# Optimization experiments

Measured on AMD Instinct MI355X. Metric: run time of the kernel, lower is better.

Reference implementation:

```python
import jax, jax.numpy as jnp
import numpy as np

B, T, NM = 128, 2048, 8  # batch, nSteps, nMaxwell


def setup_inputs() -> dict:
    key = jax.random.key(0)
    k1, k2, k3 = jax.random.split(key, 3)
    S_e = jax.random.normal(k1, (B, T, 3, 3), dtype=jnp.float32)
    # strictly increasing times per batch element
    dt = jax.random.uniform(k2, (B, T), minval=0.01, maxval=0.1, dtype=jnp.float32)
    t = jnp.cumsum(dt, axis=1)
    # [tau_1..tau_nM, g_infy, g_1..g_nM] -> last dim 2*NM + 1
    PronyParams = jax.random.uniform(k3, (B, T, 2 * NM + 1), minval=0.1, maxval=1.0, dtype=jnp.float32)
    return {"S_e": S_e, "t": t, "PronyParams": PronyParams}


def reference(S_e, t, PronyParams):
    """Viscoelastic 2nd Piola-Kirchhoff stress via recursive Prony update.

    S_e:         [B, T, 3, 3] instantaneous elastic stress
    t:           [B, T] time
    PronyParams: [B, T, 2*nM+1] (relaxation times tau then coefficients g)
    Returns (S, S_infy, Q_sum), each [B, T, 3, 3].
    """
    nM = PronyParams.shape[-1] // 2
    tau = PronyParams[..., :nM]                      # [B,T,nM]
    g = PronyParams[..., nM:]                        # [B,T,nM+1]
    g = g / jnp.sum(g, axis=-1, keepdims=True)
    g_infy = g[..., 0:1]                             # [B,T,1]
    g_i = g[..., 1:]                                 # [B,T,nM]

    Bsz = S_e.shape[0]
    # time-major scan inputs
    xs = (
        jnp.swapaxes(t, 0, 1),      # [T,B]
        jnp.swapaxes(S_e, 0, 1),    # [T,B,3,3]
        jnp.swapaxes(tau, 0, 1),    # [T,B,nM]
        jnp.swapaxes(g_i, 0, 1),    # [T,B,nM]
    )
    init = (
        jnp.zeros((Bsz, nM, 3, 3), S_e.dtype),  # Q_0
        -t[:, 1],                                # t_prev (as in original initializer)
        jnp.zeros((Bsz, 3, 3), S_e.dtype),       # S_prev
        tau[:, 0],
        g_i[:, 0],
    )

    def step(carry, x):
        Q_p, t_p, S_p, tau_p, g_p = carry
        t_c, S_c, tau_c, g_c = x
        g_bar = 0.5 * (g_c + g_p)                 # [B,nM]
        tau_bar = 0.5 * (tau_c + tau_p)           # [B,nM]
        dt = (t_c - t_p)[:, None]                 # [B,1]
        e = jnp.exp(-0.5 * dt / tau_bar)          # exp(-dt/(2 tau_bar))
        term1 = (e * e)[..., None, None]          # exp(-dt/tau_bar), [B,nM,1,1]
        term2 = (e * g_bar)[..., None, None]      # [B,nM,1,1]
        dS = (S_c - S_p)[:, None]                 # [B,1,3,3]
        Q = term1 * Q_p + term2 * dS              # [B,nM,3,3]
        return (Q, t_c, S_c, tau_c, g_c), Q

    _, Qs = jax.lax.scan(step, init, xs)          # [T,B,nM,3,3]
    Q_sum = jnp.swapaxes(jnp.sum(Qs, axis=2), 0, 1)  # [B,T,3,3]
    S_infy = g_infy[..., None] * S_e              # [B,T,1,1] * [B,T,3,3]
    S = S_infy + Q_sum
    return (S, S_infy, Q_sum)
```

## Files before the change

kernel.cpp:

```cpp
#include <hip/hip_runtime.h>

#define T_LEN 2048
#define NMODE 8
#define NPP   17

template <int L, int G>
__global__ __launch_bounds__(256, 8)
void scanK(const float* __restrict__ Se,
           const float* __restrict__ tt,
           const float* __restrict__ pp,
           float* __restrict__ out,
           float* __restrict__ caT,
           float* __restrict__ agg,
           int B) {
    constexpr int NSTEP = G * L;
    constexpr int TILES = T_LEN / NSTEP;
    constexpr int RW    = NSTEP + 1;
    constexpr int NT    = 256;
    constexpr int SROW  = NSTEP + 4;
    constexpr int QT_SZ = 9 * SROW;
    constexpr int CA_K  = L * 8 + 4;
    constexpr int AC_K  = L * 16 + 4;
    constexpr int O_AC  = QT_SZ + G * CA_K;
    constexpr int OV_ZREL = 0;
    constexpr int OV_PP   = G * 72;
    constexpr int OV_R    = OV_PP + G * 8;
    constexpr int OV_P    = OV_R + G * 72;
    static_assert(OV_P + G * 8 <= G * AC_K, "overlay fits in AC region");
    constexpr int O_INV = O_AC + G * AC_K;
    constexpr int O_GI  = O_INV + RW;
    constexpr int TOTAL = O_GI + RW;
    static_assert(TOTAL * 4 <= 20480, "LDS must allow 8 blocks/CU");
    static_assert(L == 16, "epilogue uses t>>4 / t&15");

    __shared__ __align__(16) float sm[TOTAL];
    float* s_qT   = sm;
    float* s_ca   = sm + QT_SZ;
    float* s_AC   = sm + O_AC;
    float* s_Zrel = sm + O_AC + OV_ZREL;
    float* s_Pp   = sm + O_AC + OV_PP;
    float* s_R    = sm + O_AC + OV_R;
    float* s_P    = sm + O_AC + OV_P;
    float* s_inv  = sm + O_INV;
    float* s_gi   = sm + O_GI;

    const int tid = threadIdx.x;
    const int b    = blockIdx.x / TILES;
    const int tile = blockIdx.x % TILES;

    const int base = tile * NSTEP;
    const int off  = (base == 0) ? 0 : 1;
    const int r0   = (base == 0) ? 0 : base - 1;

    const float* ppb = pp + ((size_t)b * T_LEN + r0) * NPP;
    const float* ttb = tt + (size_t)b * T_LEN + r0;

    for (int i = tid; i < RW; i += NT) {
        const float* gp = ppb + i * NPP + 8;
        float gs = 0.f;
        #pragma unroll
        for (int k = 0; k < 9; ++k) gs += gp[k];
        float iv = __builtin_amdgcn_rcpf(gs);
        s_inv[i] = iv;
        s_gi[i]  = gp[0] * iv;
    }
    __syncthreads();

    for (int i = tid; i < NSTEP * 8; i += NT) {
        int m  = i & 7;
        int ts = i >> 3;
        int rc = ts + off;
        bool first = (base == 0) && (ts == 0);
        int rp = first ? rc : rc - 1;
        float tau_c = ppb[rc * NPP + m];
        float tau_p = ppb[rp * NPP + m];
        float gqh_c = 0.5f * ppb[rc * NPP + 9 + m] * s_inv[rc];
        float gqh_p = 0.5f * ppb[rp * NPP + 9 + m] * s_inv[rp];
        float t_c = ttb[rc];
        float t_p = first ? -ttb[1] : ttb[rp];
        float ee  = __expf((t_p - t_c) * __builtin_amdgcn_rcpf(tau_c + tau_p));
        int kk = ts / L, sl = ts % L;
        s_AC[kk * AC_K + sl * 16 + m]     = ee * ee;
        s_AC[kk * AC_K + sl * 16 + 8 + m] = ee * (gqh_c + gqh_p);
    }
    __syncthreads();

    const size_t nOut = (size_t)B * T_LEN * 9;
    float* o1 = out + nOut + ((size_t)b * T_LEN + base) * 9;
    float* o2 = out + 2 * nOut + ((size_t)b * T_LEN + base) * 9;
    const float4* sv4 = (const float4*)(Se + ((size_t)b * T_LEN + base) * 9);

    float Q[8] = {0,0,0,0,0,0,0,0};
    float cumA_c = 1.f;
    if (tid < 72) {
        const int k = tid / 9;
        const int e = tid - k * 9;
        const float* Sg = Se + (size_t)b * T_LEN * 9 + e;
        const int gbase = base + k * L;

        float dS[L];
        {
            float prev = (base == 0 && k == 0) ? 0.f
                                               : Sg[(size_t)(gbase - 1) * 9];
            #pragma unroll
            for (int s = 0; s < L; ++s) {
                float cur = Sg[(size_t)(gbase + s) * 9];
                dS[s] = cur - prev;
                prev = cur;
            }
        }

        const float4* acp = (const float4*)(s_AC + k * AC_K);
        #pragma unroll
        for (int s = 0; s < L; ++s) {
            float4 a0 = acp[4*s], a1 = acp[4*s+1];
            float4 c0v = acp[4*s+2], c1v = acp[4*s+3];
            float d = dS[s];
            Q[0] = a0.x*Q[0] + c0v.x*d;  Q[1] = a0.y*Q[1] + c0v.y*d;
            Q[2] = a0.z*Q[2] + c0v.z*d;  Q[3] = a0.w*Q[3] + c0v.w*d;
            Q[4] = a1.x*Q[4] + c1v.x*d;  Q[5] = a1.y*Q[5] + c1v.y*d;
            Q[6] = a1.z*Q[6] + c1v.z*d;  Q[7] = a1.w*Q[7] + c1v.w*d;
            float qs = ((Q[0]+Q[1])+(Q[2]+Q[3])) + ((Q[4]+Q[5])+(Q[6]+Q[7]));
            s_qT[e * SROW + (k * L + s)] = qs;
        }
    } else if (tid < 192) {
        for (int i4 = tid - 72; i4 < NSTEP * 9 / 4; i4 += 120) {
            float4 sv = sv4[i4];
            int i = i4 * 4;
            float f0 = s_gi[(i    ) / 9 + off] * sv.x;
            float f1 = s_gi[(i + 1) / 9 + off] * sv.y;
            float f2 = s_gi[(i + 2) / 9 + off] * sv.z;
            float f3 = s_gi[(i + 3) / 9 + off] * sv.w;
            ((float4*)o1)[i4] = make_float4(f0, f1, f2, f3);
        }
    } else {
        const int u = tid - 192;
        const int k = u >> 3;
        const int m = u & 7;
        #pragma unroll
        for (int s = 0; s < L; ++s) {
            cumA_c *= s_AC[k * AC_K + s * 16 + m];
            s_ca[k * CA_K + s * 8 + m] = cumA_c;
        }
    }
    __syncthreads();

    if (tid < 72) {
        float4* r4 = (float4*)(s_R + 8 * tid);
        r4[0] = make_float4(Q[0], Q[1], Q[2], Q[3]);
        r4[1] = make_float4(Q[4], Q[5], Q[6], Q[7]);
    } else if (tid >= 192) {
        s_P[tid - 192] = cumA_c;
    }
    __syncthreads();

    if (tid < 72) {
        const int e = tid >> 3;
        const int m = tid & 7;
        float z = 0.f, pprod = 1.f;
        #pragma unroll
        for (int k = 0; k < G; ++k) {
            s_Zrel[k * 72 + tid] = z;
            if (e == 0) s_Pp[k * 8 + m] = pprod;
            float Pk = s_P[k * 8 + m];
            z = Pk * z + s_R[k * 72 + tid];
            pprod *= Pk;
        }
        if (tile != TILES - 1) {
            float* ap = agg + ((size_t)b * TILES + tile) * 80;
            ap[8 + tid] = z;
            if (e == 0) ap[m] = pprod;
        }
    }
    __syncthreads();

    {
        int k = tid >> 5;
        int s = (tid >> 1) & 15;
        int h = tid & 1;
        float4 cv = *(const float4*)(s_ca + k * CA_K + s * 8 + h * 4);
        float4 pv = *(const float4*)(s_Pp + k * 8 + h * 4);
        float4 ov = make_float4(cv.x*pv.x, cv.y*pv.y, cv.z*pv.z, cv.w*pv.w);
        *(float4*)(caT + (((size_t)b * T_LEN + base) + k * L + s) * 8 + h * 4)
            = ov;
    }

    for (int i4 = tid; i4 < NSTEP * 9 / 4; i4 += NT) {
        int i = i4 * 4;
        float q[4];
        #pragma unroll
        for (int j = 0; j < 4; ++j) {
            int idx = i + j;
            int t = idx / 9, e = idx - t * 9;
            int k = t >> 4, s = t & 15;
            const float4* ca4 = (const float4*)(s_ca + k * CA_K + s * 8);
            const float4* z4  = (const float4*)(s_Zrel + k * 72 + e * 8);
            float4 cA = ca4[0], cB = ca4[1];
            float4 zA = z4[0],  zB = z4[1];
            float cr = ((cA.x*zA.x + cA.y*zA.y) + (cA.z*zA.z + cA.w*zA.w))
                     + ((cB.x*zB.x + cB.y*zB.y) + (cB.z*zB.z + cB.w*zB.w));
            q[j] = s_qT[e * SROW + t] + cr;
        }
        ((float4*)o2)[i4] = make_float4(q[0], q[1], q[2], q[3]);
    }
}

template <int L, int G>
__global__ __launch_bounds__(256, 8)
void finishK(float* __restrict__ out,
             const float* __restrict__ caT,
             const float* __restrict__ agg,
             int B) {
    constexpr int NSTEP = G * L;
    constexpr int TILES = T_LEN / NSTEP;
    constexpr int NT    = 256;

    __shared__ __align__(16) float s_Z[80];
    __shared__ __align__(16) float s_ca[NSTEP * 8];

    const int tid  = threadIdx.x;
    const int b    = blockIdx.x / TILES;
    const int tile = blockIdx.x % TILES;
    const int base = tile * NSTEP;

    {
        const float4* c4 = (const float4*)(caT + ((size_t)b * T_LEN + base) * 8);
        for (int i = tid; i < NSTEP * 8 / 4; i += NT)
            ((float4*)s_ca)[i] = c4[i];
    }

    if (tid < 72) {
        const int m = tid & 7;
        float zin = 0.f;
        if (tile > 0) {
            const float* ab = agg + (size_t)b * TILES * 80;
            float Pv[TILES - 1], Rv[TILES - 1];
            #pragma unroll
            for (int j = 0; j < TILES - 1; ++j) {
                if (j < tile) {
                    Pv[j] = ab[j * 80 + m];
                    Rv[j] = ab[j * 80 + 8 + tid];
                }
            }
            #pragma unroll
            for (int j = 0; j < TILES - 1; ++j)
                if (j < tile) zin = Pv[j] * zin + Rv[j];
        }
        s_Z[tid] = zin;
    }
    __syncthreads();

    const size_t nOut = (size_t)B * T_LEN * 9;
    float* o0 = out + ((size_t)b * T_LEN + base) * 9;
    const float4* sf4 = (const float4*)(o0 + nOut);
    float4* s4 = (float4*)o0;
    float4* q4 = (float4*)(o0 + 2 * nOut);

    for (int i4 = tid; i4 < NSTEP * 9 / 4; i4 += NT) {
        float4 qv = q4[i4];
        float4 fv = sf4[i4];
        int i = i4 * 4;
        float corr[4];
        #pragma unroll
        for (int j = 0; j < 4; ++j) {
            int idx = i + j;
            int t = idx / 9, e = idx - t * 9;
            const float4* ca4 = (const float4*)(s_ca + t * 8);
            const float4* z4  = (const float4*)(s_Z + e * 8);
            float4 cA = ca4[0], cB = ca4[1];
            float4 zA = z4[0],  zB = z4[1];
            corr[j] = ((cA.x*zA.x + cA.y*zA.y) + (cA.z*zA.z + cA.w*zA.w))
                    + ((cB.x*zB.x + cB.y*zB.y) + (cB.z*zB.z + cB.w*zB.w));
        }
        float4 qn = make_float4(qv.x + corr[0], qv.y + corr[1],
                                qv.z + corr[2], qv.w + corr[3]);
        q4[i4] = qn;
        s4[i4] = make_float4(fv.x + qn.x, fv.y + qn.y,
                             fv.z + qn.z, fv.w + qn.w);
    }
}

extern "C" void kernel_launch(void* const* d_in, const int* in_sizes, int n_in,
                              void* d_out, int out_size, void* d_ws, size_t ws_size,
                              hipStream_t stream) {
    const float* Se = (const float*)d_in[0];
    const float* tt = (const float*)d_in[1];
    const float* pp = (const float*)d_in[2];
    float* out = (float*)d_out;

    int B = in_sizes[1] / T_LEN;

    constexpr int L = 16;
    constexpr int G = 8;
    constexpr int NSTEP = G * L;
    constexpr int TILES = T_LEN / NSTEP;

    float* caT = (float*)d_ws;
    float* agg = caT + (size_t)B * T_LEN * 8;

    scanK<L, G><<<B * TILES, dim3(256), 0, stream>>>(
        Se, tt, pp, out, caT, agg, B);
    finishK<L, G><<<B * TILES, dim3(256), 0, stream>>>(
        out, caT, agg, B);
}
```

Baseline: 98.73 us.

## Replace scan-then-fixup with aggregate-then-recompute two-pass scan

The first kernel now computes only per-tile aggregates (decay product and partial Q) for all tiles but the last, and writes nothing else. The second kernel takes the carry-in from those aggregates, recomputes the local scan and writes all three outputs once. This removes the caT workspace and the global round trip where the first kernel wrote Q_sum and S_infy and the second kernel read them back and rewrote them. The cost is doing the coefficient and exp computation and the local scan twice.

```diff
diff --git a/kernel.cpp b/kernel.cpp
--- a/kernel.cpp
+++ b/kernel.cpp
@@ -6,47 +6,31 @@
 
 template <int L, int G>
 __global__ __launch_bounds__(256, 8)
-void scanK(const float* __restrict__ Se,
-           const float* __restrict__ tt,
-           const float* __restrict__ pp,
-           float* __restrict__ out,
-           float* __restrict__ caT,
-           float* __restrict__ agg,
-           int B) {
+void aggK(const float* __restrict__ Se,
+          const float* __restrict__ tt,
+          const float* __restrict__ pp,
+          float* __restrict__ agg,
+          int B) {
     constexpr int NSTEP = G * L;
     constexpr int TILES = T_LEN / NSTEP;
     constexpr int RW    = NSTEP + 1;
     constexpr int NT    = 256;
-    constexpr int SROW  = NSTEP + 4;
-    constexpr int QT_SZ = 9 * SROW;
-    constexpr int CA_K  = L * 8 + 4;
     constexpr int AC_K  = L * 16 + 4;
-    constexpr int O_AC  = QT_SZ + G * CA_K;
-    constexpr int OV_ZREL = 0;
-    constexpr int OV_PP   = G * 72;
-    constexpr int OV_R    = OV_PP + G * 8;
-    constexpr int OV_P    = OV_R + G * 72;
-    static_assert(OV_P + G * 8 <= G * AC_K, "overlay fits in AC region");
-    constexpr int O_INV = O_AC + G * AC_K;
-    constexpr int O_GI  = O_INV + RW;
-    constexpr int TOTAL = O_GI + RW;
-    static_assert(TOTAL * 4 <= 20480, "LDS must allow 8 blocks/CU");
-    static_assert(L == 16, "epilogue uses t>>4 / t&15");
+    constexpr int OV_R  = 0;
+    constexpr int OV_P  = G * 72;
+    static_assert(OV_P + G * 8 <= G * AC_K, "overlay fits");
+    constexpr int O_INV = G * AC_K;
+    constexpr int TOTAL = O_INV + RW;
 
     __shared__ __align__(16) float sm[TOTAL];
-    float* s_qT   = sm;
-    float* s_ca   = sm + QT_SZ;
-    float* s_AC   = sm + O_AC;
-    float* s_Zrel = sm + O_AC + OV_ZREL;
-    float* s_Pp   = sm + O_AC + OV_PP;
-    float* s_R    = sm + O_AC + OV_R;
-    float* s_P    = sm + O_AC + OV_P;
-    float* s_inv  = sm + O_INV;
-    float* s_gi   = sm + O_GI;
-
-    const int tid = threadIdx.x;
-    const int b    = blockIdx.x / TILES;
-    const int tile = blockIdx.x % TILES;
+    float* s_AC  = sm;
+    float* s_R   = sm + OV_R;
+    float* s_P   = sm + OV_P;
+    float* s_inv = sm + O_INV;
+
+    const int tid  = threadIdx.x;
+    const int b    = blockIdx.x / (TILES - 1);
+    const int tile = blockIdx.x % (TILES - 1);
 
     const int base = tile * NSTEP;
     const int off  = (base == 0) ? 0 : 1;
@@ -60,9 +44,7 @@
         float gs = 0.f;
         #pragma unroll
         for (int k = 0; k < 9; ++k) gs += gp[k];
-        float iv = __builtin_amdgcn_rcpf(gs);
-        s_inv[i] = iv;
-        s_gi[i]  = gp[0] * iv;
+        s_inv[i] = __builtin_amdgcn_rcpf(gs);
     }
     __syncthreads();
 
@@ -85,9 +67,177 @@
     }
     __syncthreads();
 
+    float Q[8] = {0,0,0,0,0,0,0,0};
+    float cumA_c = 1.f;
+    if (tid < 72) {
+        const int k = tid / 9;
+        const int e = tid - k * 9;
+        const float* Sg = Se + (size_t)b * T_LEN * 9 + e;
+        const int gbase = base + k * L;
+
+        float dS[L];
+        {
+            float prev = (base == 0 && k == 0) ? 0.f
+                                               : Sg[(size_t)(gbase - 1) * 9];
+            #pragma unroll
+            for (int s = 0; s < L; ++s) {
+                float cur = Sg[(size_t)(gbase + s) * 9];
+                dS[s] = cur - prev;
+                prev = cur;
+            }
+        }
+
+        const float4* acp = (const float4*)(s_AC + k * AC_K);
+        #pragma unroll
+        for (int s = 0; s < L; ++s) {
+            float4 a0 = acp[4*s], a1 = acp[4*s+1];
+            float4 c0v = acp[4*s+2], c1v = acp[4*s+3];
+            float d = dS[s];
+            Q[0] = a0.x*Q[0] + c0v.x*d;  Q[1] = a0.y*Q[1] + c0v.y*d;
+            Q[2] = a0.z*Q[2] + c0v.z*d;  Q[3] = a0.w*Q[3] + c0v.w*d;
+            Q[4] = a1.x*Q[4] + c1v.x*d;  Q[5] = a1.y*Q[5] + c1v.y*d;
+            Q[6] = a1.z*Q[6] + c1v.z*d;  Q[7] = a1.w*Q[7] + c1v.w*d;
+        }
+    } else if (tid >= 192) {
+        const int u = tid - 192;
+        const int k = u >> 3;
+        const int m = u & 7;
+        #pragma unroll
+        for (int s = 0; s < L; ++s)
+            cumA_c *= s_AC[k * AC_K + s * 16 + m];
+    }
+    __syncthreads();
+
+    if (tid < 72) {
+        float4* r4 = (float4*)(s_R + 8 * tid);
+        r4[0] = make_float4(Q[0], Q[1], Q[2], Q[3]);
+        r4[1] = make_float4(Q[4], Q[5], Q[6], Q[7]);
+    } else if (tid >= 192) {
+        s_P[tid - 192] = cumA_c;
+    }
+    __syncthreads();
+
+    if (tid < 72) {
+        const int e = tid >> 3;
+        const int m = tid & 7;
+        float z = 0.f, pprod = 1.f;
+        #pragma unroll
+        for (int k = 0; k < G; ++k) {
+            float Pk = s_P[k * 8 + m];
+            z = Pk * z + s_R[k * 72 + tid];
+            pprod *= Pk;
+        }
+        float* ap = agg + ((size_t)b * TILES + tile) * 80;
+        ap[8 + tid] = z;
+        if (e == 0) ap[m] = pprod;
+    }
+}
+
+template <int L, int G>
+__global__ __launch_bounds__(256, 8)
+void finK(const float* __restrict__ Se,
+          const float* __restrict__ tt,
+          const float* __restrict__ pp,
+          float* __restrict__ out,
+          const float* __restrict__ agg,
+          int B) {
+    constexpr int NSTEP = G * L;
+    constexpr int TILES = T_LEN / NSTEP;
+    constexpr int RW    = NSTEP + 1;
+    constexpr int NT    = 256;
+    constexpr int SROW  = NSTEP + 4;
+    constexpr int QT_SZ = 9 * SROW;
+    constexpr int CA_K  = L * 8 + 4;
+    constexpr int AC_K  = L * 16 + 4;
+    constexpr int O_AC  = QT_SZ + G * CA_K;
+    constexpr int OV_R  = 0;
+    constexpr int OV_P  = G * 72;
+    constexpr int OV_Z  = OV_P + G * 8;
+    static_assert(OV_Z + G * 72 <= G * AC_K, "overlay fits");
+    constexpr int O_INV = O_AC + G * AC_K;
+    constexpr int O_GI  = O_INV + RW;
+    constexpr int O_ZIN = O_GI + RW;
+    constexpr int TOTAL = O_ZIN + 72;
+    static_assert(TOTAL * 4 <= 20480, "LDS must allow 8 blocks/CU");
+    static_assert(L == 16, "epilogue uses t>>4 / t&15");
+
+    __shared__ __align__(16) float sm[TOTAL];
+    float* s_qT  = sm;
+    float* s_ca  = sm + QT_SZ;
+    float* s_AC  = sm + O_AC;
+    float* s_R   = sm + O_AC + OV_R;
+    float* s_P   = sm + O_AC + OV_P;
+    float* s_Z   = sm + O_AC + OV_Z;
+    float* s_inv = sm + O_INV;
+    float* s_gi  = sm + O_GI;
+    float* s_Zin = sm + O_ZIN;
+
+    const int tid  = threadIdx.x;
+    const int b    = blockIdx.x / TILES;
+    const int tile = blockIdx.x % TILES;
+
+    const int base = tile * NSTEP;
+    const int off  = (base == 0) ? 0 : 1;
+    const int r0   = (base == 0) ? 0 : base - 1;
+
+    const float* ppb = pp + ((size_t)b * T_LEN + r0) * NPP;
+    const float* ttb = tt + (size_t)b * T_LEN + r0;
+
+    if (tid < 72) {
+        float zin = 0.f;
+        if (tile > 0) {
+            const int m = tid & 7;
+            const float* ab = agg + (size_t)b * TILES * 80;
+            float Pv[TILES - 1], Rv[TILES - 1];
+            #pragma unroll
+            for (int j = 0; j < TILES - 1; ++j) {
+                if (j < tile) {
+                    Pv[j] = ab[j * 80 + m];
+                    Rv[j] = ab[j * 80 + 8 + tid];
+                }
+            }
+            #pragma unroll
+            for (int j = 0; j < TILES - 1; ++j)
+                if (j < tile) zin = Pv[j] * zin + Rv[j];
+        }
+        s_Zin[tid] = zin;
+    } else {
+        int i = tid - 72;
+        if (i < RW) {
+            const float* gp = ppb + i * NPP + 8;
+            float gs = 0.f;
+            #pragma unroll
+            for (int k = 0; k < 9; ++k) gs += gp[k];
+            float iv = __builtin_amdgcn_rcpf(gs);
+            s_inv[i] = iv;
+            s_gi[i]  = gp[0] * iv;
+        }
+    }
+    __syncthreads();
+
+    for (int i = tid; i < NSTEP * 8; i += NT) {
+        int m  = i & 7;
+        int ts = i >> 3;
+        int rc = ts + off;
+        bool first = (base == 0) && (ts == 0);
+        int rp = first ? rc : rc - 1;
+        float tau_c = ppb[rc * NPP + m];
+        float tau_p = ppb[rp * NPP + m];
+        float gqh_c = 0.5f * ppb[rc * NPP + 9 + m] * s_inv[rc];
+        float gqh_p = 0.5f * ppb[rp * NPP + 9 + m] * s_inv[rp];
+        float t_c = ttb[rc];
+        float t_p = first ? -ttb[1] : ttb[rp];
+        float ee  = __expf((t_p - t_c) * __builtin_amdgcn_rcpf(tau_c + tau_p));
+        int kk = ts / L, sl = ts % L;
+        s_AC[kk * AC_K + sl * 16 + m]     = ee * ee;
+        s_AC[kk * AC_K + sl * 16 + 8 + m] = ee * (gqh_c + gqh_p);
+    }
+    __syncthreads();
+
     const size_t nOut = (size_t)B * T_LEN * 9;
-    float* o1 = out + nOut + ((size_t)b * T_LEN + base) * 9;
-    float* o2 = out + 2 * nOut + ((size_t)b * T_LEN + base) * 9;
+    float* o0 = out + ((size_t)b * T_LEN + base) * 9;
+    float* o1 = o0 + nOut;
+    float* o2 = o0 + 2 * nOut;
     const float4* sv4 = (const float4*)(Se + ((size_t)b * T_LEN + base) * 9);
 
     float Q[8] = {0,0,0,0,0,0,0,0};
@@ -155,128 +305,39 @@
     __syncthreads();
 
     if (tid < 72) {
-        const int e = tid >> 3;
         const int m = tid & 7;
-        float z = 0.f, pprod = 1.f;
+        float z = s_Zin[tid];
         #pragma unroll
         for (int k = 0; k < G; ++k) {
-            s_Zrel[k * 72 + tid] = z;
-            if (e == 0) s_Pp[k * 8 + m] = pprod;
-            float Pk = s_P[k * 8 + m];
-            z = Pk * z + s_R[k * 72 + tid];
-            pprod *= Pk;
-        }
-        if (tile != TILES - 1) {
-            float* ap = agg + ((size_t)b * TILES + tile) * 80;
-            ap[8 + tid] = z;
-            if (e == 0) ap[m] = pprod;
-        }
-    }
-    __syncthreads();
-
-    {
-        int k = tid >> 5;
-        int s = (tid >> 1) & 15;
-        int h = tid & 1;
-        float4 cv = *(const float4*)(s_ca + k * CA_K + s * 8 + h * 4);
-        float4 pv = *(const float4*)(s_Pp + k * 8 + h * 4);
-        float4 ov = make_float4(cv.x*pv.x, cv.y*pv.y, cv.z*pv.z, cv.w*pv.w);
-        *(float4*)(caT + (((size_t)b * T_LEN + base) + k * L + s) * 8 + h * 4)
-            = ov;
-    }
+            s_Z[k * 72 + tid] = z;
+            z = s_P[k * 8 + m] * z + s_R[k * 72 + tid];
+        }
+    }
+    __syncthreads();
 
     for (int i4 = tid; i4 < NSTEP * 9 / 4; i4 += NT) {
+        float4 sv = sv4[i4];
+        const float svc[4] = {sv.x, sv.y, sv.z, sv.w};
         int i = i4 * 4;
-        float q[4];
+        float q[4], f[4];
         #pragma unroll
         for (int j = 0; j < 4; ++j) {
             int idx = i + j;
             int t = idx / 9, e = idx - t * 9;
+            int rc = t + off;
             int k = t >> 4, s = t & 15;
             const float4* ca4 = (const float4*)(s_ca + k * CA_K + s * 8);
-            const float4* z4  = (const float4*)(s_Zrel + k * 72 + e * 8);
+            const float4* z4  = (const float4*)(s_Z + k * 72 + e * 8);
             float4 cA = ca4[0], cB = ca4[1];
             float4 zA = z4[0],  zB = z4[1];
             float cr = ((cA.x*zA.x + cA.y*zA.y) + (cA.z*zA.z + cA.w*zA.w))
                      + ((cB.x*zB.x + cB.y*zB.y) + (cB.z*zB.z + cB.w*zB.w));
             q[j] = s_qT[e * SROW + t] + cr;
+            f[j] = s_gi[rc] * svc[j];
         }
         ((float4*)o2)[i4] = make_float4(q[0], q[1], q[2], q[3]);
-    }
-}
-
-template <int L, int G>
-__global__ __launch_bounds__(256, 8)
-void finishK(float* __restrict__ out,
-             const float* __restrict__ caT,
-             const float* __restrict__ agg,
-             int B) {
-    constexpr int NSTEP = G * L;
-    constexpr int TILES = T_LEN / NSTEP;
-    constexpr int NT    = 256;
-
-    __shared__ __align__(16) float s_Z[80];
-    __shared__ __align__(16) float s_ca[NSTEP * 8];
-
-    const int tid  = threadIdx.x;
-    const int b    = blockIdx.x / TILES;
-    const int tile = blockIdx.x % TILES;
-    const int base = tile * NSTEP;
-
-    {
-        const float4* c4 = (const float4*)(caT + ((size_t)b * T_LEN + base) * 8);
-        for (int i = tid; i < NSTEP * 8 / 4; i += NT)
-            ((float4*)s_ca)[i] = c4[i];
-    }
-
-    if (tid < 72) {
-        const int m = tid & 7;
-        float zin = 0.f;
-        if (tile > 0) {
-            const float* ab = agg + (size_t)b * TILES * 80;
-            float Pv[TILES - 1], Rv[TILES - 1];
-            #pragma unroll
-            for (int j = 0; j < TILES - 1; ++j) {
-                if (j < tile) {
-                    Pv[j] = ab[j * 80 + m];
-                    Rv[j] = ab[j * 80 + 8 + tid];
-                }
-            }
-            #pragma unroll
-            for (int j = 0; j < TILES - 1; ++j)
-                if (j < tile) zin = Pv[j] * zin + Rv[j];
-        }
-        s_Z[tid] = zin;
-    }
-    __syncthreads();
-
-    const size_t nOut = (size_t)B * T_LEN * 9;
-    float* o0 = out + ((size_t)b * T_LEN + base) * 9;
-    const float4* sf4 = (const float4*)(o0 + nOut);
-    float4* s4 = (float4*)o0;
-    float4* q4 = (float4*)(o0 + 2 * nOut);
-
-    for (int i4 = tid; i4 < NSTEP * 9 / 4; i4 += NT) {
-        float4 qv = q4[i4];
-        float4 fv = sf4[i4];
-        int i = i4 * 4;
-        float corr[4];
-        #pragma unroll
-        for (int j = 0; j < 4; ++j) {
-            int idx = i + j;
-            int t = idx / 9, e = idx - t * 9;
-            const float4* ca4 = (const float4*)(s_ca + t * 8);
-            const float4* z4  = (const float4*)(s_Z + e * 8);
-            float4 cA = ca4[0], cB = ca4[1];
-            float4 zA = z4[0],  zB = z4[1];
-            corr[j] = ((cA.x*zA.x + cA.y*zA.y) + (cA.z*zA.z + cA.w*zA.w))
-                    + ((cB.x*zB.x + cB.y*zB.y) + (cB.z*zB.z + cB.w*zB.w));
-        }
-        float4 qn = make_float4(qv.x + corr[0], qv.y + corr[1],
-                                qv.z + corr[2], qv.w + corr[3]);
-        q4[i4] = qn;
-        s4[i4] = make_float4(fv.x + qn.x, fv.y + qn.y,
-                             fv.z + qn.z, fv.w + qn.w);
+        ((float4*)o0)[i4] = make_float4(f[0]+q[0], f[1]+q[1],
+                                        f[2]+q[2], f[3]+q[3]);
     }
 }
 
@@ -295,11 +356,10 @@
     constexpr int NSTEP = G * L;
     constexpr int TILES = T_LEN / NSTEP;
 
-    float* caT = (float*)d_ws;
-    float* agg = caT + (size_t)B * T_LEN * 8;
-
-    scanK<L, G><<<B * TILES, dim3(256), 0, stream>>>(
-        Se, tt, pp, out, caT, agg, B);
-    finishK<L, G><<<B * TILES, dim3(256), 0, stream>>>(
-        out, caT, agg, B);
+    float* agg = (float*)d_ws;
+
+    aggK<L, G><<<B * (TILES - 1), dim3(256), 0, stream>>>(
+        Se, tt, pp, agg, B);
+    finK<L, G><<<B * TILES, dim3(256), 0, stream>>>(
+        Se, tt, pp, out, agg, B);
 }
```

Result: no change. 99.62 us (+0.9%).
